# Kernel optimization log

Measured on AMD Instinct MI355X. Metric: run time of the kernel, lower is better.

## Reference

```python
import jax, jax.numpy as jnp
import numpy as np

EPS = 1e-5
KS = 3
PAD = 1


def _bn(x, g, b, m, v):
    inv = g / jnp.sqrt(v + EPS)
    return x * inv[None, :, None, None] + (b - m * inv)[None, :, None, None]


def _deform_conv2d(x, off_w, off_b, w):
    # x: (B,C,H,W); off_w: (2*9,C,3,3); w: (Cout,C,3,3)
    B, C, H, W = x.shape
    N = KS * KS
    off = jax.lax.conv_general_dilated(x, off_w, (1, 1), ((PAD, PAD), (PAD, PAD)))
    off = off + off_b[None, :, None, None]                      # (B,2N,H,W)
    xp = jnp.pad(x, ((0, 0), (0, 0), (PAD, PAD), (PAD, PAD)))
    Hp, Wp = H + 2 * PAD, W + 2 * PAD
    r = jnp.arange(KS, dtype=x.dtype) - (KS - 1) // 2           # kernel offsets
    pny = jnp.repeat(r, KS)                                     # row-major (dy)
    pnx = jnp.tile(r, KS)                                       # row-major (dx)
    p0y = jnp.arange(1, H + 1, dtype=x.dtype)[None, None, :, None]
    p0x = jnp.arange(1, W + 1, dtype=x.dtype)[None, None, None, :]
    py = off[:, :N] + pny[None, :, None, None] + p0y            # (B,N,H,W)
    px = off[:, N:] + pnx[None, :, None, None] + p0x
    py = jnp.clip(py, 0.0, Hp - 1.0)
    px = jnp.clip(px, 0.0, Wp - 1.0)
    fy = jax.lax.stop_gradient(jnp.floor(py))                   # indices detached (as in torch impl)
    fx = jax.lax.stop_gradient(jnp.floor(px))
    qy0 = jnp.clip(fy, 0.0, Hp - 1.0)
    qx0 = jnp.clip(fx, 0.0, Wp - 1.0)
    qy1 = jnp.clip(fy + 1.0, 0.0, Hp - 1.0)
    qx1 = jnp.clip(fx + 1.0, 0.0, Wp - 1.0)
    xf = xp.reshape(B, C, Hp * Wp)

    def gather(qy, qx):
        idx = (qy * Wp + qx).astype(jnp.int32)                  # (B,N,H,W)
        return jax.vmap(lambda m_, i_: m_[:, i_])(xf, idx)       # (B,C,N,H,W)

    g_lt = (1.0 + (qy0 - py)) * (1.0 + (qx0 - px))
    g_rb = (1.0 - (qy1 - py)) * (1.0 - (qx1 - px))
    g_lb = (1.0 + (qy0 - py)) * (1.0 - (qx1 - px))
    g_rt = (1.0 - (qy1 - py)) * (1.0 + (qx0 - px))
    xo = (g_lt[:, None] * gather(qy0, qx0) + g_rb[:, None] * gather(qy1, qx1)
          + g_lb[:, None] * gather(qy0, qx1) + g_rt[:, None] * gather(qy1, qx0))
    # (B,C,N,H,W) -> (B,C,H*KS,W*KS): N = (row, col) row-major
    xo = xo.reshape(B, C, KS, KS, H, W).transpose(0, 1, 4, 2, 5, 3).reshape(B, C, H * KS, W * KS)
    return jax.lax.conv_general_dilated(xo, w, (KS, KS), 'VALID')


def _forward(x, dc1_offw, dc1_offb, dc1_w, bn1_g, bn1_b, bn1_m, bn1_v,
             dc2_offw, dc2_offb, dc2_w, bn2_g, bn2_b, bn2_m, bn2_v,
             id_w, id_b, bn3_g, bn3_b, bn3_m, bn3_v):
    h = jax.nn.relu(_bn(_deform_conv2d(x, dc1_offw, dc1_offb, dc1_w), bn1_g, bn1_b, bn1_m, bn1_v))
    h = _bn(_deform_conv2d(h, dc2_offw, dc2_offb, dc2_w), bn2_g, bn2_b, bn2_m, bn2_v)
    idt = jnp.einsum('bchw,oc->bohw', x, id_w[:, :, 0, 0]) + id_b[None, :, None, None]
    idt = _bn(idt, bn3_g, bn3_b, bn3_m, bn3_v)
    return jax.nn.relu(h + idt)


def setup_inputs() -> dict:
    key = jax.random.key(0)
    ks = jax.random.split(key, 16)
    B, Cin, Cout, H, W = 2, 64, 128, 128, 128
    N2 = 2 * KS * KS
    d = {}
    d['x'] = jax.random.normal(ks[0], (B, Cin, H, W), jnp.float32)
    d['dc1_offw'] = jax.random.normal(ks[1], (N2, Cin, KS, KS), jnp.float32) * 0.01
    d['dc1_offb'] = jnp.zeros((N2,), jnp.float32)
    d['dc1_w'] = jax.random.normal(ks[2], (Cout, Cin, KS, KS), jnp.float32) * 0.05
    d['bn1_g'] = 1.0 + 0.1 * jax.random.normal(ks[3], (Cout,), jnp.float32)
    d['bn1_b'] = 0.1 * jax.random.normal(ks[4], (Cout,), jnp.float32)
    d['bn1_m'] = 0.1 * jax.random.normal(ks[5], (Cout,), jnp.float32)
    d['bn1_v'] = jnp.ones((Cout,), jnp.float32)
    d['dc2_offw'] = jax.random.normal(ks[6], (N2, Cout, KS, KS), jnp.float32) * 0.01
    d['dc2_offb'] = jnp.zeros((N2,), jnp.float32)
    d['dc2_w'] = jax.random.normal(ks[7], (Cout, Cout, KS, KS), jnp.float32) * 0.03
    d['bn2_g'] = 1.0 + 0.1 * jax.random.normal(ks[8], (Cout,), jnp.float32)
    d['bn2_b'] = 0.1 * jax.random.normal(ks[9], (Cout,), jnp.float32)
    d['bn2_m'] = 0.1 * jax.random.normal(ks[10], (Cout,), jnp.float32)
    d['bn2_v'] = jnp.ones((Cout,), jnp.float32)
    d['id_w'] = jax.random.normal(ks[11], (Cout, Cin, 1, 1), jnp.float32) * 0.1
    d['id_b'] = jnp.zeros((Cout,), jnp.float32)
    d['bn3_g'] = 1.0 + 0.1 * jax.random.normal(ks[12], (Cout,), jnp.float32)
    d['bn3_b'] = 0.1 * jax.random.normal(ks[13], (Cout,), jnp.float32)
    d['bn3_m'] = 0.1 * jax.random.normal(ks[14], (Cout,), jnp.float32)
    d['bn3_v'] = jnp.ones((Cout,), jnp.float32)
    return d


def reference(x, dc1_offw, dc1_offb, dc1_w, bn1_g, bn1_b, bn1_m, bn1_v,
              dc2_offw, dc2_offb, dc2_w, bn2_g, bn2_b, bn2_m, bn2_v,
              id_w, id_b, bn3_g, bn3_b, bn3_m, bn3_v):
    return _forward(x, dc1_offw, dc1_offb, dc1_w, bn1_g, bn1_b, bn1_m, bn1_v,
                    dc2_offw, dc2_offb, dc2_w, bn2_g, bn2_b, bn2_m, bn2_v,
                    id_w, id_b, bn3_g, bn3_b, bn3_m, bn3_v)
```

## Files before the change

### kernel.cpp

```cpp
#include <hip/hip_runtime.h>
#include <math.h>

#define HH 128
#define WW 128
#define HWSZ (HH * WW)
#define BB 2
#define COUT 128

typedef __bf16 bf16x8 __attribute__((ext_vector_type(8)));
typedef float f32x4 __attribute__((ext_vector_type(4)));
typedef float f32x2 __attribute__((ext_vector_type(2)));
typedef short s16x8 __attribute__((ext_vector_type(8)));
typedef short s16x4 __attribute__((ext_vector_type(4)));
typedef unsigned short u16x4 __attribute__((ext_vector_type(4)));
typedef unsigned short u16x8 __attribute__((ext_vector_type(8)));

__device__ __forceinline__ short tobf(float f) {
  union { float f; unsigned u; } v; v.f = f;
  unsigned r = v.u + 0x7fffu + ((v.u >> 16) & 1u);
  return (short)(r >> 16);
}
__device__ __forceinline__ float asf(unsigned u) {
  union { unsigned u; float f; } v; v.u = u;
  return v.f;
}
__device__ __forceinline__ f32x2 up2(unsigned u) {
  f32x2 r; r[0] = asf(u << 16); r[1] = asf(u & 0xffff0000u); return r;
}
__device__ __forceinline__ unsigned trunc2bf(f32x2 v) {
  union { float f; unsigned u; } a, b;
  a.f = v[0]; b.f = v[1];
  return __builtin_amdgcn_perm(b.u, a.u, 0x07060302u);
}

#define PA0 73728
#define PA1 221184
#define PA2 229376
#define PA3 247808
#define PA4 284672
#define PA5 284928
__global__ __launch_bounds__(256) void prep_all_kernel(
    const float* __restrict__ dc1_w, const float* __restrict__ dc2_w,
    const float* __restrict__ id_w, const float* __restrict__ dc1_offw,
    const float* __restrict__ dc2_offw,
    const float* g1, const float* b1, const float* m1, const float* v1,
    const float* g2, const float* b2, const float* m2, const float* v2,
    const float* g3, const float* b3, const float* m3, const float* v3,
    const float* idb,
    short* __restrict__ wbf1, short* __restrict__ wbf2,
    short* __restrict__ woff1, short* __restrict__ woff2,
    float* __restrict__ cb1, float* __restrict__ cb2) {
  int idx = blockIdx.x * 256 + threadIdx.x;
  if (idx < PA0) {
    int o = idx / 576, k = idx - o * 576;
    float inv = g1[o] / sqrtf(v1[o] + 1e-5f);
    int col = (k % 9) * 64 + k / 9;
    int di = (((col >> 5) * 2 + (o >> 6)) * 4 + ((o >> 4) & 3)) * 512
           + (((o & 15) | (((col >> 3) & 3) << 4)) * 8) + (col & 7);
    wbf1[di] = tobf(dc1_w[(size_t)o * 576 + k] * inv);
  } else if (idx < PA1) {
    int j = idx - PA0;
    int o = j / 1152, k = j - o * 1152;
    float inv = g2[o] / sqrtf(v2[o] + 1e-5f);
    int col = (k % 9) * 128 + k / 9;
    int di = (((col >> 5) * 2 + (o >> 6)) * 4 + ((o >> 4) & 3)) * 512
           + (((o & 15) | (((col >> 3) & 3) << 4)) * 8) + (col & 7);
    wbf2[di] = tobf(dc2_w[(size_t)o * 1152 + k] * inv);
  } else if (idx < PA2) {
    int j = idx - PA1;
    int o = j >> 6, k = j & 63;
    float inv = g3[o] / sqrtf(v3[o] + 1e-5f);
    int col = 1152 + k;
    int di = (((col >> 5) * 2 + (o >> 6)) * 4 + ((o >> 4) & 3)) * 512
           + (((o & 15) | (((col >> 3) & 3) << 4)) * 8) + (col & 7);
    wbf2[di] = tobf(id_w[(size_t)o * 64 + k] * inv);
  } else if (idx < PA3) {
    int j = idx - PA2;
    int o = j / 576, k = j - o * 576;
    int col = (k % 9) * 64 + k / 9;
    int di = ((col >> 5) * 2 + (o >> 4)) * 512 + ((col >> 3) & 3) * 128
           + (o & 15) * 8 + (col & 7);
    woff1[di] = (o < 18) ? tobf(dc1_offw[(size_t)o * 576 + k]) : (short)0;
  } else if (idx < PA4) {
    int j = idx - PA3;
    int o = j / 1152, k = j - o * 1152;
    int col = (k % 9) * 128 + k / 9;
    int di = ((col >> 5) * 2 + (o >> 4)) * 512 + ((col >> 3) & 3) * 128
           + (o & 15) * 8 + (col & 7);
    woff2[di] = (o < 18) ? tobf(dc2_offw[(size_t)o * 1152 + k]) : (short)0;
  } else if (idx < PA5) {
    int j = idx - PA4;
    if (j < 128) {
      float inv = g1[j] / sqrtf(v1[j] + 1e-5f);
      cb1[j] = b1[j] - m1[j] * inv;
    } else {
      int o = j - 128;
      float inv2_ = g2[o] / sqrtf(v2[o] + 1e-5f);
      float inv3_ = g3[o] / sqrtf(v3[o] + 1e-5f);
      cb2[o] = (b2[o] - m2[o] * inv2_) + idb[o] * inv3_ + (b3[o] - m3[o] * inv3_);
    }
  }
}

__global__ __launch_bounds__(256) void xcast_kernel(const float* __restrict__ x,
                                                    unsigned short* __restrict__ xn) {
  __shared__ short lds[64 * 72];
  int tid = threadIdx.x;
  int gp0 = blockIdx.x * 64;
  int b = gp0 >> 14;
  int pl0 = gp0 & 16383;
  int p = tid & 63;
  int cb = (tid >> 6) * 16;
#pragma unroll
  for (int i = 0; i < 16; i++) {
    int c = cb + i;
    lds[p * 72 + c] = tobf(x[((size_t)(b * 64 + c)) * HWSZ + pl0 + p]);
  }
  __syncthreads();
  int pw = tid >> 2, cseg = (tid & 3) * 16;
  u16x8 a = *(const u16x8*)&lds[pw * 72 + cseg];
  u16x8 b8 = *(const u16x8*)&lds[pw * 72 + cseg + 8];
  *(u16x8*)&xn[(size_t)(gp0 + pw) * 64 + cseg] = a;
  *(u16x8*)&xn[(size_t)(gp0 + pw) * 64 + cseg + 8] = b8;
}

#define LOADW(P, kc_)                                           \
  {                                                             \
    const short* wf_ = wfb + (size_t)(kc_) * 4096;              \
    P##w0 = *(const bf16x8*)(wf_);                              \
    P##w1 = *(const bf16x8*)(wf_ + 512);                        \
    P##w2 = *(const bf16x8*)(wf_ + 1024);                       \
    P##w3 = *(const bf16x8*)(wf_ + 1536);                       \
    P##w4 = *(const bf16x8*)(wf_ + 2048);                       \
    P##w5 = *(const bf16x8*)(wf_ + 2560);                       \
    P##w6 = *(const bf16x8*)(wf_ + 3072);                       \
    P##w7 = *(const bf16x8*)(wf_ + 3584);                       \
  }

#define LOADT(P, kc_)                                           \
  {                                                             \
    int k0_ = (kc_) << 5;                                       \
    int n_ = k0_ >> CSH;                                        \
    int c0_ = (k0_ & (Cin - 1)) + cq * 8;                       \
    uint4 d4_ = dsu[(n_ << 6) + dp0];                           \
    int dx_ = (int)(d4_.w & 0xffffu);                           \
    int dy_ = (int)d4_.w >> 16;                                 \
    const unsigned short* p_ = inb + (int)d4_.z + c0_;          \
    P##q00 = *(const uint4*)(p_);                               \
    P##q01 = *(const uint4*)(p_ + dx_);                         \
    P##q02 = *(const uint4*)(p_ + dy_);                         \
    P##q03 = *(const uint4*)(p_ + dx_ + dy_);                   \
    P##wa0 = d4_.x; P##wb0 = d4_.y;                             \
    uint4 e4_ = dsu[(n_ << 6) + dp1];                           \
    int ex_ = (int)(e4_.w & 0xffffu);                           \
    int ey_ = (int)e4_.w >> 16;                                 \
    const unsigned short* q_ = inb + (int)e4_.z + c0_;          \
    P##q10 = *(const uint4*)(q_);                               \
    P##q11 = *(const uint4*)(q_ + ex_);                         \
    P##q12 = *(const uint4*)(q_ + ey_);                         \
    P##q13 = *(const uint4*)(q_ + ex_ + ey_);                   \
    P##wa1 = e4_.x; P##wb1 = e4_.y;                             \
  }

#define BLEND1(r0, r1, r2, r3, wav, wbv, pkv)                                 \
  {                                                                           \
    float w0_ = asf((wav) << 16), w1_ = asf((wav) & 0xffff0000u);             \
    float w2_ = asf((wbv) << 16), w3_ = asf((wbv) & 0xffff0000u);             \
    f32x2 v0_ = up2(r0.x) * w0_ + up2(r1.x) * w1_                             \
              + up2(r2.x) * w2_ + up2(r3.x) * w3_;                            \
    f32x2 v1_ = up2(r0.y) * w0_ + up2(r1.y) * w1_                             \
              + up2(r2.y) * w2_ + up2(r3.y) * w3_;                            \
    f32x2 v2_ = up2(r0.z) * w0_ + up2(r1.z) * w1_                             \
              + up2(r2.z) * w2_ + up2(r3.z) * w3_;                            \
    f32x2 v3_ = up2(r0.w) * w0_ + up2(r1.w) * w1_                             \
              + up2(r2.w) * w2_ + up2(r3.w) * w3_;                            \
    pkv.x = trunc2bf(v0_); pkv.y = trunc2bf(v1_);                             \
    pkv.z = trunc2bf(v2_); pkv.w = trunc2bf(v3_);                             \
  }

#define XPOSE(pkv, bfrv)                                                      \
  {                                                                           \
    union { int i[4]; bf16x8 v; } bu_;                                        \
    bu_.i[0] = __builtin_amdgcn_ds_bpermute(baddr, (int)pkv.x);               \
    bu_.i[1] = __builtin_amdgcn_ds_bpermute(baddr, (int)pkv.y);               \
    bu_.i[2] = __builtin_amdgcn_ds_bpermute(baddr, (int)pkv.z);               \
    bu_.i[3] = __builtin_amdgcn_ds_bpermute(baddr, (int)pkv.w);               \
    bfrv = bu_.v;                                                             \
  }

#define MFMA16(P, bfr0v, bfr1v)                                                     \
  {                                                                                 \
    acc[0] = __builtin_amdgcn_mfma_f32_16x16x32_bf16(P##w0, bfr0v, acc[0], 0, 0, 0);  \
    acc[8] = __builtin_amdgcn_mfma_f32_16x16x32_bf16(P##w0, bfr1v, acc[8], 0, 0, 0);  \
    acc[1] = __builtin_amdgcn_mfma_f32_16x16x32_bf16(P##w1, bfr0v, acc[1], 0, 0, 0);  \
    acc[9] = __builtin_amdgcn_mfma_f32_16x16x32_bf16(P##w1, bfr1v, acc[9], 0, 0, 0);  \
    acc[2] = __builtin_amdgcn_mfma_f32_16x16x32_bf16(P##w2, bfr0v, acc[2], 0, 0, 0);  \
    acc[10] = __builtin_amdgcn_mfma_f32_16x16x32_bf16(P##w2, bfr1v, acc[10], 0, 0, 0);\
    acc[3] = __builtin_amdgcn_mfma_f32_16x16x32_bf16(P##w3, bfr0v, acc[3], 0, 0, 0);  \
    acc[11] = __builtin_amdgcn_mfma_f32_16x16x32_bf16(P##w3, bfr1v, acc[11], 0, 0, 0);\
    acc[4] = __builtin_amdgcn_mfma_f32_16x16x32_bf16(P##w4, bfr0v, acc[4], 0, 0, 0);  \
    acc[12] = __builtin_amdgcn_mfma_f32_16x16x32_bf16(P##w4, bfr1v, acc[12], 0, 0, 0);\
    acc[5] = __builtin_amdgcn_mfma_f32_16x16x32_bf16(P##w5, bfr0v, acc[5], 0, 0, 0);  \
    acc[13] = __builtin_amdgcn_mfma_f32_16x16x32_bf16(P##w5, bfr1v, acc[13], 0, 0, 0);\
    acc[6] = __builtin_amdgcn_mfma_f32_16x16x32_bf16(P##w6, bfr0v, acc[6], 0, 0, 0);  \
    acc[14] = __builtin_amdgcn_mfma_f32_16x16x32_bf16(P##w6, bfr1v, acc[14], 0, 0, 0);\
    acc[7] = __builtin_amdgcn_mfma_f32_16x16x32_bf16(P##w7, bfr0v, acc[7], 0, 0, 0);  \
    acc[15] = __builtin_amdgcn_mfma_f32_16x16x32_bf16(P##w7, bfr1v, acc[15], 0, 0, 0);\
  }

#define COMPUTE(P)                                                            \
  {                                                                           \
    uint4 pk0_, pk1_;                                                         \
    BLEND1(P##q00, P##q01, P##q02, P##q03, P##wa0, P##wb0, pk0_);             \
    BLEND1(P##q10, P##q11, P##q12, P##q13, P##wa1, P##wb1, pk1_);             \
    bf16x8 bf0_, bf1_;                                                        \
    XPOSE(pk0_, bf0_);                                                        \
    XPOSE(pk1_, bf1_);                                                        \
    MFMA16(P, bf0_, bf1_);                                                    \
  }

template <int CSH, int KCONV, int KTOT, int MODE>
__global__ __launch_bounds__(256, 2) void fused_layer_kernel(
    const unsigned short* __restrict__ in, const short* __restrict__ woff,
    const float* __restrict__ offb,
    const short* __restrict__ wbf, const float* __restrict__ cbv,
    const unsigned short* __restrict__ xid, float* __restrict__ outf,
    unsigned short* __restrict__ outb) {
  __shared__ __align__(16) char smem[50176];
  uint4* dsu = (uint4*)smem;
  f32x4* redf = (f32x4*)smem;
  float* offlds = (float*)(smem + 32768);
  short* trans = (short*)(smem + 32768);

  const int tid = threadIdx.x;
  const int lane = tid & 63, wv = tid >> 6;
  const int pb = ((blockIdx.x & 7) << 6) | (blockIdx.x >> 3);
  const int pix0 = pb << 6;
  const int x0 = pix0 & 127, y = (pix0 >> 7) & 127, b = pix0 >> 14;
  constexpr int Cin = 1 << CSH;
  const unsigned short* inb = in + (size_t)b * HWSZ * Cin;
  const int l15 = lane & 15, quad = lane >> 4;
  const int pxg = wv & 1, kh = wv >> 1;
  const int dp0 = pxg * 32 + (lane >> 2);
  const int dp1 = dp0 + 16;
  const int cq = lane & 3;
  const int baddr = (((lane & 15) << 2) | (lane >> 4)) << 2;

  {
    constexpr int NCh = (9 << CSH) >> 5;
    const int pxa = wv;
    const int px = x0 + pxa * 16 + l15;
    f32x4 aco0 = {0.f, 0.f, 0.f, 0.f};
    f32x4 aco1 = {0.f, 0.f, 0.f, 0.f};
#pragma unroll
    for (int i = 0; i < NCh; i++) {
      int k0 = i * 32;
      int n = k0 >> CSH;
      int c0 = (k0 & (Cin - 1)) + quad * 8;
      int yy = y + n / 3 - 1;
      int xx = px + n % 3 - 1;
      bf16x8 bv = {};
      if (((unsigned)yy < (unsigned)HH) && ((unsigned)xx < (unsigned)WW))
        bv = *(const bf16x8*)&inb[((size_t)yy * WW + xx) * Cin + c0];
      int fbase = i * 1024 + lane * 8;
      bf16x8 a0 = *(const bf16x8*)&woff[fbase];
      bf16x8 a1 = *(const bf16x8*)&woff[fbase + 512];
      aco0 = __builtin_amdgcn_mfma_f32_16x16x32_bf16(a0, bv, aco0, 0, 0, 0);
      aco1 = __builtin_amdgcn_mfma_f32_16x16x32_bf16(a1, bv, aco1, 0, 0, 0);
    }
#pragma unroll
    for (int r = 0; r < 4; r++) {
      int o0 = quad * 4 + r;
      offlds[o0 * 64 + pxa * 16 + l15] = aco0[r] + offb[o0];
      int o1 = 16 + quad * 4 + r;
      if (o1 < 18)
        offlds[o1 * 64 + pxa * 16 + l15] = aco1[r] + offb[o1];
    }
  }

  bf16x8 Aw0, Aw1, Aw2, Aw3, Aw4, Aw5, Aw6, Aw7;
  bf16x8 Bw0, Bw1, Bw2, Bw3, Bw4, Bw5, Bw6, Bw7;
  uint4 Aq00, Aq01, Aq02, Aq03, Aq10, Aq11, Aq12, Aq13;
  uint4 Bq00, Bq01, Bq02, Bq03, Bq10, Bq11, Bq12, Bq13;
  unsigned Awa0, Awb0, Awa1, Awb1, Bwa0, Bwb0, Bwa1, Bwb1;

  constexpr int NC = KTOT >> 5;
  constexpr int NCONV = KCONV >> 5;
  constexpr int HC = NC >> 1;
  const int kcBeg = kh * HC;
  const int kcEnd = kcBeg + HC;
  const int kcEndConv = (kcEnd < NCONV) ? kcEnd : NCONV;
  const short* wfb = wbf + lane * 8;

  LOADW(A, kcBeg);
  __syncthreads();

  for (int t = tid; t < 576; t += 256) {
    int n = t >> 6, pp = t & 63;
    float offy = offlds[n * 64 + pp];
    float offx = offlds[(9 + n) * 64 + pp];
    float py = offy + (float)(n / 3 - 1) + (float)(y + 1);
    float px = offx + (float)(n % 3 - 1) + (float)(x0 + pp + 1);
    py = fminf(fmaxf(py, 0.f), 129.f);
    px = fminf(fmaxf(px, 0.f), 129.f);
    float fy = floorf(py), fx = floorf(px);
    float qy1 = fminf(fy + 1.f, 129.f), qx1 = fminf(fx + 1.f, 129.f);
    float ty0 = 1.f + fy - py, ty1 = 1.f - (qy1 - py);
    float tx0 = 1.f + fx - px, tx1 = 1.f - (qx1 - px);
    int iy0 = (int)fy - 1, ix0 = (int)fx - 1;
    int iy1 = (int)qy1 - 1, ix1 = (int)qx1 - 1;
    if ((unsigned)iy0 >= (unsigned)HH) ty0 = 0.f;
    if ((unsigned)iy1 >= (unsigned)HH) ty1 = 0.f;
    if ((unsigned)ix0 >= (unsigned)WW) tx0 = 0.f;
    if ((unsigned)ix1 >= (unsigned)WW) tx1 = 0.f;
    int by0 = min(max(iy0, 0), HH - 1), by1 = min(max(iy1, 0), HH - 1);
    int bx0 = min(max(ix0, 0), WW - 1), bx1 = min(max(ix1, 0), WW - 1);
    uint4 d4;
    d4.x = (unsigned)(unsigned short)tobf(ty0 * tx0)
         | ((unsigned)(unsigned short)tobf(ty0 * tx1) << 16);
    d4.y = (unsigned)(unsigned short)tobf(ty1 * tx0)
         | ((unsigned)(unsigned short)tobf(ty1 * tx1) << 16);
    d4.z = (unsigned)((by0 * WW + bx0) * Cin);
    d4.w = (unsigned)((((by1 - by0) * WW * Cin) << 16) | ((bx1 - bx0) * Cin));
    dsu[t] = d4;
  }

  f32x4 acc[16];
#pragma unroll
  for (int j = 0; j < 16; j++) acc[j] = (f32x4){0.f, 0.f, 0.f, 0.f};

  __syncthreads();

  LOADT(A, kcBeg);
  int i = kcBeg;
  for (; i + 2 <= kcEndConv; i += 2) {
    LOADW(B, i + 1);
    LOADT(B, i + 1);
    COMPUTE(A);
    if (i + 2 < kcEndConv) {
      LOADW(A, i + 2);
      LOADT(A, i + 2);
    }
    COMPUTE(B);
  }
  if (i < kcEndConv) {
    COMPUTE(A);
    i++;
  }

  if (KCONV < KTOT) {
    for (; i < kcEnd; i++) {
      LOADW(A, i);
      int c = ((i << 5) - KCONV) + cq * 8;
      uint4 pk0 = *(const uint4*)&xid[((size_t)(b * HWSZ) + y * WW + x0 + dp0) * 64 + c];
      uint4 pk1 = *(const uint4*)&xid[((size_t)(b * HWSZ) + y * WW + x0 + dp1) * 64 + c];
      bf16x8 bf0, bf1;
      XPOSE(pk0, bf0);
      XPOSE(pk1, bf1);
      MFMA16(A, bf0, bf1);
    }
  }

  __syncthreads();
  if (kh == 1) {
#pragma unroll
    for (int f = 0; f < 16; f++) redf[f * 128 + pxg * 64 + lane] = acc[f];
  }
  __syncthreads();
  if (kh == 0) {
#pragma unroll
    for (int f = 0; f < 16; f++) acc[f] += redf[f * 128 + pxg * 64 + lane];
    if (MODE == 1) {
#pragma unroll
      for (int f = 0; f < 16; f++) {
        int px_ = x0 + pxg * 32 + (f >> 3) * 16 + l15;
        int fo = f & 7;
#pragma unroll
        for (int r = 0; r < 4; r++) {
          int o = (fo >> 2) * 64 + (fo & 3) * 16 + quad * 4 + r;
          outf[(size_t)(b * COUT + o) * HWSZ + y * WW + px_] =
              fmaxf(acc[f][r] + cbv[o], 0.f);
        }
      }
    } else {
#pragma unroll
      for (int f = 0; f < 16; f++) {
        int pl = pxg * 32 + (f >> 3) * 16 + l15;
        int fo = f & 7;
        s16x4 t4;
#pragma unroll
        for (int r = 0; r < 4; r++) {
          int o = (fo >> 2) * 64 + (fo & 3) * 16 + quad * 4 + r;
          t4[r] = tobf(fmaxf(acc[f][r] + cbv[o], 0.f));
        }
        *(s16x4*)&trans[pl * 136 + (fo >> 2) * 64 + (fo & 3) * 16 + quad * 4] = t4;
      }
    }
  }
  if (MODE == 0) {
    __syncthreads();
    int pw = tid >> 2, cs = (tid & 3) * 32;
    size_t gb = ((size_t)(b * HWSZ) + y * WW + x0 + pw) * 128 + cs;
#pragma unroll
    for (int s = 0; s < 4; s++) {
      u16x8 v8 = *(const u16x8*)&trans[pw * 136 + cs + s * 8];
      *(u16x8*)&outb[gb + s * 8] = v8;
    }
  }
}

extern "C" void kernel_launch(void* const* d_in, const int* in_sizes, int n_in,
                              void* d_out, int out_size, void* d_ws, size_t ws_size,
                              hipStream_t stream) {
  const float* x        = (const float*)d_in[0];
  const float* dc1_offw = (const float*)d_in[1];
  const float* dc1_offb = (const float*)d_in[2];
  const float* dc1_w    = (const float*)d_in[3];
  const float* bn1_g    = (const float*)d_in[4];
  const float* bn1_b    = (const float*)d_in[5];
  const float* bn1_m    = (const float*)d_in[6];
  const float* bn1_v    = (const float*)d_in[7];
  const float* dc2_offw = (const float*)d_in[8];
  const float* dc2_offb = (const float*)d_in[9];
  const float* dc2_w    = (const float*)d_in[10];
  const float* bn2_g    = (const float*)d_in[11];
  const float* bn2_b    = (const float*)d_in[12];
  const float* bn2_m    = (const float*)d_in[13];
  const float* bn2_v    = (const float*)d_in[14];
  const float* id_w     = (const float*)d_in[15];
  const float* id_b     = (const float*)d_in[16];
  const float* bn3_g    = (const float*)d_in[17];
  const float* bn3_b    = (const float*)d_in[18];
  const float* bn3_m    = (const float*)d_in[19];
  const float* bn3_v    = (const float*)d_in[20];

  float* wsf = (float*)d_ws;
  float* cb1  = wsf;
  float* cb2  = cb1 + 128;
  unsigned short* xbf = (unsigned short*)(cb2 + 128);
  unsigned short* h1  = xbf + (size_t)BB * HWSZ * 64;
  short* wbf1  = (short*)(h1 + (size_t)BB * HWSZ * COUT);
  short* wbf2  = wbf1 + (size_t)128 * 576;
  short* woff1 = wbf2 + (size_t)128 * 1216;
  short* woff2 = woff1 + (size_t)18 * 1024;

  hipLaunchKernelGGL(prep_all_kernel, dim3((PA5 + 255) / 256), dim3(256), 0, stream,
                     dc1_w, dc2_w, id_w, dc1_offw, dc2_offw,
                     bn1_g, bn1_b, bn1_m, bn1_v, bn2_g, bn2_b, bn2_m, bn2_v,
                     bn3_g, bn3_b, bn3_m, bn3_v, id_b,
                     wbf1, wbf2, woff1, woff2, cb1, cb2);
  hipLaunchKernelGGL(xcast_kernel, dim3(BB * HWSZ / 64), dim3(256), 0, stream, x, xbf);

  hipLaunchKernelGGL((fused_layer_kernel<6, 576, 576, 0>), dim3(512), dim3(256), 0, stream,
                     xbf, woff1, dc1_offb, wbf1, cb1,
                     (const unsigned short*)nullptr, (float*)nullptr, h1);
  hipLaunchKernelGGL((fused_layer_kernel<7, 1152, 1216, 1>), dim3(512), dim3(256), 0, stream,
                     h1, woff2, dc2_offb, wbf2, cb2,
                     xbf, (float*)d_out, (unsigned short*)nullptr);
}
```

Baseline: 174.5 us.

## Triple-buffer gather loads, single-buffer weights, and raise priority around MFMA blocks

Restructures the main deformable-conv loop from a two-stage A/B ping-pong into a three-stage rotation. The gathered input taps are prefetched two K-chunks ahead, while the weight fragments are kept in a single register set reloaded right after each MFMA block. It adds sched_barrier to keep the prefetch ahead of compute and s_setprio around MFMA issue to favour matrix work across waves. This trades weight-register space for a deeper gather pipeline that hides global-load latency. The weight loads are now exposed with less lead time, and register pressure may still affect the 2-waves-per-SIMD occupancy.

```diff
diff --git a/kernel.cpp b/kernel.cpp
--- a/kernel.cpp
+++ b/kernel.cpp
@@ -124,17 +124,17 @@
   *(u16x8*)&xn[(size_t)(gp0 + pw) * 64 + cseg + 8] = b8;
 }
 
-#define LOADW(P, kc_)                                           \
+#define LOADW1(kc_)                                             \
   {                                                             \
     const short* wf_ = wfb + (size_t)(kc_) * 4096;              \
-    P##w0 = *(const bf16x8*)(wf_);                              \
-    P##w1 = *(const bf16x8*)(wf_ + 512);                        \
-    P##w2 = *(const bf16x8*)(wf_ + 1024);                       \
-    P##w3 = *(const bf16x8*)(wf_ + 1536);                       \
-    P##w4 = *(const bf16x8*)(wf_ + 2048);                       \
-    P##w5 = *(const bf16x8*)(wf_ + 2560);                       \
-    P##w6 = *(const bf16x8*)(wf_ + 3072);                       \
-    P##w7 = *(const bf16x8*)(wf_ + 3584);                       \
+    w0 = *(const bf16x8*)(wf_);                                 \
+    w1 = *(const bf16x8*)(wf_ + 512);                           \
+    w2 = *(const bf16x8*)(wf_ + 1024);                          \
+    w3 = *(const bf16x8*)(wf_ + 1536);                          \
+    w4 = *(const bf16x8*)(wf_ + 2048);                          \
+    w5 = *(const bf16x8*)(wf_ + 2560);                          \
+    w6 = *(const bf16x8*)(wf_ + 3072);                          \
+    w7 = *(const bf16x8*)(wf_ + 3584);                          \
   }
 
 #define LOADT(P, kc_)                                           \
@@ -188,27 +188,27 @@
     bfrv = bu_.v;                                                             \
   }
 
-#define MFMA16(P, bfr0v, bfr1v)                                                     \
+#define MFMA16(bfr0v, bfr1v)                                                        \
   {                                                                                 \
-    acc[0] = __builtin_amdgcn_mfma_f32_16x16x32_bf16(P##w0, bfr0v, acc[0], 0, 0, 0);  \
-    acc[8] = __builtin_amdgcn_mfma_f32_16x16x32_bf16(P##w0, bfr1v, acc[8], 0, 0, 0);  \
-    acc[1] = __builtin_amdgcn_mfma_f32_16x16x32_bf16(P##w1, bfr0v, acc[1], 0, 0, 0);  \
-    acc[9] = __builtin_amdgcn_mfma_f32_16x16x32_bf16(P##w1, bfr1v, acc[9], 0, 0, 0);  \
-    acc[2] = __builtin_amdgcn_mfma_f32_16x16x32_bf16(P##w2, bfr0v, acc[2], 0, 0, 0);  \
-    acc[10] = __builtin_amdgcn_mfma_f32_16x16x32_bf16(P##w2, bfr1v, acc[10], 0, 0, 0);\
-    acc[3] = __builtin_amdgcn_mfma_f32_16x16x32_bf16(P##w3, bfr0v, acc[3], 0, 0, 0);  \
-    acc[11] = __builtin_amdgcn_mfma_f32_16x16x32_bf16(P##w3, bfr1v, acc[11], 0, 0, 0);\
-    acc[4] = __builtin_amdgcn_mfma_f32_16x16x32_bf16(P##w4, bfr0v, acc[4], 0, 0, 0);  \
-    acc[12] = __builtin_amdgcn_mfma_f32_16x16x32_bf16(P##w4, bfr1v, acc[12], 0, 0, 0);\
-    acc[5] = __builtin_amdgcn_mfma_f32_16x16x32_bf16(P##w5, bfr0v, acc[5], 0, 0, 0);  \
-    acc[13] = __builtin_amdgcn_mfma_f32_16x16x32_bf16(P##w5, bfr1v, acc[13], 0, 0, 0);\
-    acc[6] = __builtin_amdgcn_mfma_f32_16x16x32_bf16(P##w6, bfr0v, acc[6], 0, 0, 0);  \
-    acc[14] = __builtin_amdgcn_mfma_f32_16x16x32_bf16(P##w6, bfr1v, acc[14], 0, 0, 0);\
-    acc[7] = __builtin_amdgcn_mfma_f32_16x16x32_bf16(P##w7, bfr0v, acc[7], 0, 0, 0);  \
-    acc[15] = __builtin_amdgcn_mfma_f32_16x16x32_bf16(P##w7, bfr1v, acc[15], 0, 0, 0);\
-  }
-
-#define COMPUTE(P)                                                            \
+    acc[0] = __builtin_amdgcn_mfma_f32_16x16x32_bf16(w0, bfr0v, acc[0], 0, 0, 0);   \
+    acc[8] = __builtin_amdgcn_mfma_f32_16x16x32_bf16(w0, bfr1v, acc[8], 0, 0, 0);   \
+    acc[1] = __builtin_amdgcn_mfma_f32_16x16x32_bf16(w1, bfr0v, acc[1], 0, 0, 0);   \
+    acc[9] = __builtin_amdgcn_mfma_f32_16x16x32_bf16(w1, bfr1v, acc[9], 0, 0, 0);   \
+    acc[2] = __builtin_amdgcn_mfma_f32_16x16x32_bf16(w2, bfr0v, acc[2], 0, 0, 0);   \
+    acc[10] = __builtin_amdgcn_mfma_f32_16x16x32_bf16(w2, bfr1v, acc[10], 0, 0, 0); \
+    acc[3] = __builtin_amdgcn_mfma_f32_16x16x32_bf16(w3, bfr0v, acc[3], 0, 0, 0);   \
+    acc[11] = __builtin_amdgcn_mfma_f32_16x16x32_bf16(w3, bfr1v, acc[11], 0, 0, 0); \
+    acc[4] = __builtin_amdgcn_mfma_f32_16x16x32_bf16(w4, bfr0v, acc[4], 0, 0, 0);   \
+    acc[12] = __builtin_amdgcn_mfma_f32_16x16x32_bf16(w4, bfr1v, acc[12], 0, 0, 0); \
+    acc[5] = __builtin_amdgcn_mfma_f32_16x16x32_bf16(w5, bfr0v, acc[5], 0, 0, 0);   \
+    acc[13] = __builtin_amdgcn_mfma_f32_16x16x32_bf16(w5, bfr1v, acc[13], 0, 0, 0); \
+    acc[6] = __builtin_amdgcn_mfma_f32_16x16x32_bf16(w6, bfr0v, acc[6], 0, 0, 0);   \
+    acc[14] = __builtin_amdgcn_mfma_f32_16x16x32_bf16(w6, bfr1v, acc[14], 0, 0, 0); \
+    acc[7] = __builtin_amdgcn_mfma_f32_16x16x32_bf16(w7, bfr0v, acc[7], 0, 0, 0);   \
+    acc[15] = __builtin_amdgcn_mfma_f32_16x16x32_bf16(w7, bfr1v, acc[15], 0, 0, 0); \
+  }
+
+#define COMPUTEB(P)                                                           \
   {                                                                           \
     uint4 pk0_, pk1_;                                                         \
     BLEND1(P##q00, P##q01, P##q02, P##q03, P##wa0, P##wb0, pk0_);             \
@@ -216,7 +216,18 @@
     bf16x8 bf0_, bf1_;                                                        \
     XPOSE(pk0_, bf0_);                                                        \
     XPOSE(pk1_, bf1_);                                                        \
-    MFMA16(P, bf0_, bf1_);                                                    \
+    __builtin_amdgcn_s_setprio(1);                                            \
+    MFMA16(bf0_, bf1_);                                                       \
+    __builtin_amdgcn_s_setprio(0);                                            \
+  }
+
+#define STEP(CUR, NX2)                                                        \
+  {                                                                           \
+    if (i + 2 < kcEndConv) { LOADT(NX2, i + 2); }                             \
+    __builtin_amdgcn_sched_barrier(0);                                        \
+    COMPUTEB(CUR);                                                            \
+    ++i;                                                                      \
+    if (i < kcEndConv) LOADW1(i);                                             \
   }
 
 template <int CSH, int KCONV, int KTOT, int MODE>
@@ -278,11 +289,13 @@
     }
   }
 
-  bf16x8 Aw0, Aw1, Aw2, Aw3, Aw4, Aw5, Aw6, Aw7;
-  bf16x8 Bw0, Bw1, Bw2, Bw3, Bw4, Bw5, Bw6, Bw7;
+  bf16x8 w0, w1, w2, w3, w4, w5, w6, w7;
   uint4 Aq00, Aq01, Aq02, Aq03, Aq10, Aq11, Aq12, Aq13;
   uint4 Bq00, Bq01, Bq02, Bq03, Bq10, Bq11, Bq12, Bq13;
-  unsigned Awa0, Awb0, Awa1, Awb1, Bwa0, Bwb0, Bwa1, Bwb1;
+  uint4 Cq00, Cq01, Cq02, Cq03, Cq10, Cq11, Cq12, Cq13;
+  unsigned Awa0, Awb0, Awa1, Awb1;
+  unsigned Bwa0, Bwb0, Bwa1, Bwb1;
+  unsigned Cwa0, Cwb0, Cwa1, Cwb1;
 
   constexpr int NC = KTOT >> 5;
   constexpr int NCONV = KCONV >> 5;
@@ -292,7 +305,7 @@
   const int kcEndConv = (kcEnd < NCONV) ? kcEnd : NCONV;
   const short* wfb = wbf + lane * 8;
 
-  LOADW(A, kcBeg);
+  LOADW1(kcBeg);
   __syncthreads();
 
   for (int t = tid; t < 576; t += 256) {
@@ -331,33 +344,32 @@
 
   __syncthreads();
 
-  LOADT(A, kcBeg);
   int i = kcBeg;
-  for (; i + 2 <= kcEndConv; i += 2) {
-    LOADW(B, i + 1);
-    LOADT(B, i + 1);
-    COMPUTE(A);
-    if (i + 2 < kcEndConv) {
-      LOADW(A, i + 2);
-      LOADT(A, i + 2);
-    }
-    COMPUTE(B);
-  }
   if (i < kcEndConv) {
-    COMPUTE(A);
-    i++;
+    LOADT(A, i);
+    if (i + 1 < kcEndConv) LOADT(B, i + 1);
+    while (true) {
+      STEP(A, C);
+      if (i >= kcEndConv) break;
+      STEP(B, A);
+      if (i >= kcEndConv) break;
+      STEP(C, B);
+      if (i >= kcEndConv) break;
+    }
   }
 
   if (KCONV < KTOT) {
     for (; i < kcEnd; i++) {
-      LOADW(A, i);
+      LOADW1(i);
       int c = ((i << 5) - KCONV) + cq * 8;
       uint4 pk0 = *(const uint4*)&xid[((size_t)(b * HWSZ) + y * WW + x0 + dp0) * 64 + c];
       uint4 pk1 = *(const uint4*)&xid[((size_t)(b * HWSZ) + y * WW + x0 + dp1) * 64 + c];
       bf16x8 bf0, bf1;
       XPOSE(pk0, bf0);
       XPOSE(pk1, bf1);
-      MFMA16(A, bf0, bf1);
+      __builtin_amdgcn_s_setprio(1);
+      MFMA16(bf0, bf1);
+      __builtin_amdgcn_s_setprio(0);
     }
   }
 
```

After: 244.5 us. +40.1%, slower.
